# Kernel optimization log

Measured on AMD Instinct MI355X. Metric: run time of the kernel, lower is better.

Reference implementation:

```python
import math
import jax, jax.numpy as jnp
import numpy as np

H, DK = 16, 64            # n_heads, d_kv
NUM_BUCKETS, MAX_DIST = 32, 128


def _relative_position_buckets(S):
    # Bidirectional (encoder) T5 bucketization of relative positions.
    ctx = jnp.arange(S, dtype=jnp.int32)[:, None]      # query positions
    mem = jnp.arange(S, dtype=jnp.int32)[None, :]      # key positions
    rp = mem - ctx                                     # [S, S]
    nb = NUM_BUCKETS // 2
    rb = (rp > 0).astype(jnp.int32) * nb
    n = jnp.abs(rp)
    max_exact = nb // 2
    is_small = n < max_exact
    large = max_exact + (
        jnp.log(jnp.maximum(n, 1).astype(jnp.float32) / max_exact)
        / math.log(MAX_DIST / max_exact)
        * (nb - max_exact)
    ).astype(jnp.int32)
    large = jnp.minimum(large, nb - 1)
    return rb + jnp.where(is_small, n, large)          # [S, S] int32


def setup_inputs() -> dict:
    key = jax.random.key(0)
    ks = jax.random.split(key, 6)
    B, S, D = 4, 1024, 1024
    inner = H * DK
    std = 0.02
    return {
        "hidden_states": jax.random.normal(ks[0], (B, S, D), jnp.float32),
        "Wq": jax.random.normal(ks[1], (inner, D), jnp.float32) * std,
        "Wk": jax.random.normal(ks[2], (inner, D), jnp.float32) * std,
        "Wv": jax.random.normal(ks[3], (inner, D), jnp.float32) * std,
        "Wo": jax.random.normal(ks[4], (D, inner), jnp.float32) * std,
        "rel_bias": jax.random.normal(ks[5], (NUM_BUCKETS, H), jnp.float32) * std,
    }


def reference(hidden_states, Wq, Wk, Wv, Wo, rel_bias):
    B, S, D = hidden_states.shape

    def proj(W):  # bias-free linear + split heads -> [B, H, S, DK]
        return (hidden_states @ W.T).reshape(B, S, H, DK).transpose(0, 2, 1, 3)

    q, k, v = proj(Wq), proj(Wk), proj(Wv)
    # T5: NO 1/sqrt(d) scaling
    scores = jnp.einsum("bhqd,bhkd->bhqk", q, k)       # [B, H, S, S]
    bias = rel_bias[_relative_position_buckets(S)]     # [S, S, H]
    scores = scores + bias.transpose(2, 0, 1)[None]    # broadcast over batch
    attn = jax.nn.softmax(scores, axis=-1)
    ctx = jnp.einsum("bhqk,bhkd->bhqd", attn, v)       # [B, H, S, DK]
    ctx = ctx.transpose(0, 2, 1, 3).reshape(B, S, H * DK)
    return ctx @ Wo.T                                  # [B, S, D]
```

## Files before the change

kernel.cpp:

```cpp
#include <hip/hip_runtime.h>

typedef _Float16 half8 __attribute__((ext_vector_type(8)));
typedef _Float16 half4_t __attribute__((ext_vector_type(4)));
typedef float f32x4 __attribute__((ext_vector_type(4)));

#define GK 1024
#define MEG (1024 * 1024)
#define LOG2E 1.44269504088896f

#define GLD16(gptr, lptr) \
    __builtin_amdgcn_global_load_lds((const __attribute__((address_space(1))) void*)(gptr), \
                                     (__attribute__((address_space(3))) void*)(lptr), 16, 0, 0)

__global__ void cvt_all_kernel(const float* __restrict__ hidden,
                               const float* __restrict__ Wq,
                               const float* __restrict__ Wk,
                               const float* __restrict__ Wv,
                               const float* __restrict__ Wo,
                               _Float16* __restrict__ ws) {
    int b = blockIdx.x;
    const float* src;
    _Float16* dst;
    if (b < 4096)      { src = hidden; dst = ws; }
    else if (b < 5120) { src = Wq; dst = ws + 4 * MEG; b -= 4096; }
    else if (b < 6144) { src = Wk; dst = ws + 5 * MEG; b -= 5120; }
    else if (b < 7168) { src = Wv; dst = ws + 6 * MEG; b -= 6144; }
    else               { src = Wo; dst = ws + 7 * MEG; b -= 7168; }
    int i = (b * 256 + threadIdx.x) * 4;
    f32x4 v = *(const f32x4*)(src + i);
    half4_t h;
    h[0] = (_Float16)v[0]; h[1] = (_Float16)v[1];
    h[2] = (_Float16)v[2]; h[3] = (_Float16)v[3];
    *(half4_t*)(dst + i) = h;
}

__global__ __launch_bounds__(256) void gemm_qkv_kernel(
    const _Float16* __restrict__ A,
    const _Float16* __restrict__ B0,
    const _Float16* __restrict__ B1,
    const _Float16* __restrict__ B2,
    _Float16* __restrict__ O0,
    _Float16* __restrict__ O1,
    _Float16* __restrict__ O2)
{
    int z = blockIdx.z;
    const _Float16* Bw = (z == 0) ? B0 : ((z == 1) ? B1 : B2);
    _Float16* Oh = (z == 0) ? O0 : ((z == 1) ? O1 : O2);

    __shared__ __attribute__((aligned(16))) _Float16 sA[2][128][32];
    __shared__ __attribute__((aligned(16))) _Float16 sB[2][128][32];

    const int tid = threadIdx.x;
    const int wave = tid >> 6, lane = tid & 63;
    const int quad = lane >> 4, l16 = lane & 15;
    const int wr = wave >> 1, wc = wave & 1;
    const int M0 = blockIdx.y * 128, N0 = blockIdx.x * 128;

    const int rl = lane >> 2;
    const int cl = (lane & 3) * 8;
    const size_t aRow0 = (size_t)(M0 + wave * 16 + rl) * GK + cl;
    const size_t aRow1 = aRow0 + (size_t)64 * GK;
    const size_t bRow0 = (size_t)(N0 + wave * 16 + rl) * GK + cl;
    const size_t bRow1 = bRow0 + (size_t)64 * GK;
    _Float16* ldsA[2][2] = {{&sA[0][wave * 16][0], &sA[0][64 + wave * 16][0]},
                            {&sA[1][wave * 16][0], &sA[1][64 + wave * 16][0]}};
    _Float16* ldsB[2][2] = {{&sB[0][wave * 16][0], &sB[0][64 + wave * 16][0]},
                            {&sB[1][wave * 16][0], &sB[1][64 + wave * 16][0]}};

    f32x4 acc[4][4] = {};

    for (int kt = 0; kt < GK / 64; ++kt) {
        const int ko = kt * 64;
        #pragma unroll
        for (int c = 0; c < 2; ++c) {
            GLD16(A + aRow0 + ko + c * 32, ldsA[c][0]);
            GLD16(A + aRow1 + ko + c * 32, ldsA[c][1]);
            GLD16(Bw + bRow0 + ko + c * 32, ldsB[c][0]);
            GLD16(Bw + bRow1 + ko + c * 32, ldsB[c][1]);
        }
        __syncthreads();
        #pragma unroll
        for (int c = 0; c < 2; ++c) {
            half8 af[4], bf[4];
            #pragma unroll
            for (int i = 0; i < 4; ++i)
                af[i] = *(const half8*)&sA[c][wr * 64 + i * 16 + l16][quad * 8];
            #pragma unroll
            for (int j = 0; j < 4; ++j)
                bf[j] = *(const half8*)&sB[c][wc * 64 + j * 16 + l16][quad * 8];
            #pragma unroll
            for (int i = 0; i < 4; ++i)
                #pragma unroll
                for (int j = 0; j < 4; ++j)
                    acc[i][j] = __builtin_amdgcn_mfma_f32_16x16x32_f16(af[i], bf[j], acc[i][j], 0, 0, 0);
        }
        __syncthreads();
    }

    #pragma unroll
    for (int i = 0; i < 4; ++i) {
        #pragma unroll
        for (int j = 0; j < 4; ++j) {
            #pragma unroll
            for (int r = 0; r < 4; ++r) {
                int m = M0 + wr * 64 + i * 16 + quad * 4 + r;
                int n = N0 + wc * 64 + j * 16 + l16;
                int b = m >> 10, s = m & 1023, hh = n >> 6, d = n & 63;
                Oh[((size_t)((b * 16 + hh) * 1024 + s)) * 64 + d] = (_Float16)acc[i][j][r];
            }
        }
    }
}

__global__ __launch_bounds__(256) void gemm_o_kernel(
    const _Float16* __restrict__ A,
    const _Float16* __restrict__ Bw,
    float* __restrict__ Of)
{
    __shared__ __attribute__((aligned(16))) _Float16 sA[2][64][32];
    __shared__ __attribute__((aligned(16))) _Float16 sB[2][128][32];

    const int tid = threadIdx.x;
    const int wave = tid >> 6, lane = tid & 63;
    const int quad = lane >> 4, l16 = lane & 15;
    const int M0 = blockIdx.y * 64, N0 = blockIdx.x * 128;

    const int rl = lane >> 2;
    const int cl = (lane & 3) * 8;
    const size_t aRow  = (size_t)(M0 + wave * 16 + rl) * GK + cl;
    const size_t bRow0 = (size_t)(N0 + wave * 16 + rl) * GK + cl;
    const size_t bRow1 = bRow0 + (size_t)64 * GK;
    _Float16* ldsA[2]    = {&sA[0][wave * 16][0], &sA[1][wave * 16][0]};
    _Float16* ldsB[2][2] = {{&sB[0][wave * 16][0], &sB[0][64 + wave * 16][0]},
                            {&sB[1][wave * 16][0], &sB[1][64 + wave * 16][0]}};

    f32x4 acc[4][2] = {};

    for (int kt = 0; kt < GK / 64; ++kt) {
        const int ko = kt * 64;
        #pragma unroll
        for (int c = 0; c < 2; ++c) {
            GLD16(A + aRow + ko + c * 32, ldsA[c]);
            GLD16(Bw + bRow0 + ko + c * 32, ldsB[c][0]);
            GLD16(Bw + bRow1 + ko + c * 32, ldsB[c][1]);
        }
        __syncthreads();
        #pragma unroll
        for (int c = 0; c < 2; ++c) {
            half8 af[4], bf[2];
            #pragma unroll
            for (int i = 0; i < 4; ++i)
                af[i] = *(const half8*)&sA[c][i * 16 + l16][quad * 8];
            #pragma unroll
            for (int j = 0; j < 2; ++j)
                bf[j] = *(const half8*)&sB[c][wave * 32 + j * 16 + l16][quad * 8];
            #pragma unroll
            for (int i = 0; i < 4; ++i)
                #pragma unroll
                for (int j = 0; j < 2; ++j)
                    acc[i][j] = __builtin_amdgcn_mfma_f32_16x16x32_f16(af[i], bf[j], acc[i][j], 0, 0, 0);
        }
        __syncthreads();
    }

    #pragma unroll
    for (int i = 0; i < 4; ++i) {
        #pragma unroll
        for (int j = 0; j < 2; ++j) {
            #pragma unroll
            for (int r = 0; r < 4; ++r) {
                int m = M0 + i * 16 + quad * 4 + r;
                int n = N0 + wave * 32 + j * 16 + l16;
                Of[(size_t)m * 1024 + n] = acc[i][j][r];
            }
        }
    }
}

__global__ __launch_bounds__(256) void transpose_v_kernel(
    const _Float16* __restrict__ V, _Float16* __restrict__ VT) {
    __shared__ _Float16 tile[64][65];
    const int s0 = blockIdx.x * 64;
    const int bh = blockIdx.y;
    const _Float16* Vb = V + (size_t)bh * 1024 * 64;
    _Float16* Tb = VT + (size_t)bh * 64 * 1024;
    const int tr = threadIdx.x >> 6;
    const int tc = threadIdx.x & 63;
    #pragma unroll
    for (int i = 0; i < 16; ++i) {
        int r = i * 4 + tr;
        tile[r][tc] = Vb[(size_t)(s0 + r) * 64 + tc];
    }
    __syncthreads();
    #pragma unroll
    for (int i = 0; i < 16; ++i) {
        int d = i * 4 + tr;
        Tb[(size_t)d * 1024 + s0 + tc] = tile[tc][d];
    }
}

__global__ __launch_bounds__(256) void attn_kernel(
    const _Float16* __restrict__ Q,
    const _Float16* __restrict__ K,
    const _Float16* __restrict__ VT,
    const float* __restrict__ rel_bias,
    _Float16* __restrict__ ctx)
{
    const int S = 1024;
    const int qt = blockIdx.x;
    const int q0 = qt * 64;
    const int h = blockIdx.y;
    const int b = blockIdx.z;
    const int bh = b * 16 + h;
    const _Float16* Qh = Q + (size_t)bh * S * 64;
    const _Float16* Kh = K + (size_t)bh * S * 64;
    const _Float16* VTh = VT + (size_t)bh * 64 * S;

    __shared__ __attribute__((aligned(16))) _Float16 sQ[64][72];
    __shared__ __attribute__((aligned(16))) _Float16 sK[64][72];
    __shared__ __attribute__((aligned(16))) _Float16 sVt[64][72];
    __shared__ __attribute__((aligned(16))) _Float16 sP[4][16][72];
    __shared__ _Float16 sBias[1088];

    const int tid = threadIdx.x;
    const int wave = tid >> 6, lane = tid & 63;
    const int quad = lane >> 4, l16 = lane & 15;

    {
        int r = tid >> 3, c = (tid & 7) * 8;
        *(half8*)&sQ[r][c]      = *(const half8*)(Qh + (size_t)(q0 + r) * 64 + c);
        *(half8*)&sQ[r + 32][c] = *(const half8*)(Qh + (size_t)(q0 + r + 32) * 64 + c);
    }
    for (int i = tid; i < 1087; i += 256) {
        int delta = i - (q0 + 63);
        int rb = (delta > 0) ? 16 : 0;
        int n = (delta < 0) ? -delta : delta;
        int bucket;
        if (n < 8) bucket = rb + n;
        else bucket = rb + 8 + (n >= 12) + (n >= 16) + (n >= 23) + (n >= 32)
                             + (n >= 46) + (n >= 64) + (n >= 91);
        sBias[i] = (_Float16)rel_bias[bucket * 16 + h];
    }
    __syncthreads();

    half8 qf0 = *(const half8*)&sQ[wave * 16 + l16][quad * 8];
    half8 qf1 = *(const half8*)&sQ[wave * 16 + l16][32 + quad * 8];

    const int sr = tid >> 3;
    const int sc_ = (tid & 7) * 8;
    const _Float16* kp0 = Kh + (size_t)sr * 64 + sc_;
    const _Float16* kp1 = kp0 + (size_t)32 * 64;
    const _Float16* vp0 = VTh + (size_t)sr * S + sc_;
    const _Float16* vp1 = vp0 + (size_t)32 * S;
    _Float16* sKw0 = &sK[sr][sc_];
    _Float16* sKw1 = &sK[sr + 32][sc_];
    _Float16* sVw0 = &sVt[sr][sc_];
    _Float16* sVw1 = &sVt[sr + 32][sc_];

    half8 rk0 = *(const half8*)kp0;
    half8 rk1 = *(const half8*)kp1;
    half8 rv0 = *(const half8*)vp0;
    half8 rv1 = *(const half8*)vp1;
    kp0 += 4096; kp1 += 4096; vp0 += 64; vp1 += 64;

    float m_run = -INFINITY, l_run = 0.0f;
    f32x4 acc[4] = {};

    for (int kt = 0; kt < 16; ++kt) {
        __syncthreads();
        *(half8*)sKw0 = rk0;
        *(half8*)sKw1 = rk1;
        *(half8*)sVw0 = rv0;
        *(half8*)sVw1 = rv1;
        __syncthreads();
        if (kt < 15) {
            rk0 = *(const half8*)kp0;
            rk1 = *(const half8*)kp1;
            rv0 = *(const half8*)vp0;
            rv1 = *(const half8*)vp1;
            kp0 += 4096; kp1 += 4096; vp0 += 64; vp1 += 64;
        }

        f32x4 sc[4] = {};
        #pragma unroll
        for (int j = 0; j < 4; ++j) {
            half8 kf0 = *(const half8*)&sK[j * 16 + l16][quad * 8];
            half8 kf1 = *(const half8*)&sK[j * 16 + l16][32 + quad * 8];
            sc[j] = __builtin_amdgcn_mfma_f32_16x16x32_f16(kf0, qf0, sc[j], 0, 0, 0);
            sc[j] = __builtin_amdgcn_mfma_f32_16x16x32_f16(kf1, qf1, sc[j], 0, 0, 0);
        }

        const int bbase = kt * 64 + quad * 4 - wave * 16 - l16 + 63;
        float ps = 0.0f;
        if (kt <= qt - 3 || kt >= qt + 3) {
            const float cb = (float)sBias[bbase];
            float mx = fmaxf(fmaxf(fmaxf(sc[0][0], sc[0][1]), fmaxf(sc[0][2], sc[0][3])),
                             fmaxf(fmaxf(sc[1][0], sc[1][1]), fmaxf(sc[1][2], sc[1][3])));
            mx = fmaxf(mx, fmaxf(fmaxf(fmaxf(sc[2][0], sc[2][1]), fmaxf(sc[2][2], sc[2][3])),
                                 fmaxf(fmaxf(sc[3][0], sc[3][1]), fmaxf(sc[3][2], sc[3][3]))));
            mx = fmaxf(mx, __shfl_xor(mx, 16));
            mx = fmaxf(mx, __shfl_xor(mx, 32));
            float mnew = fmaxf(m_run, mx + cb);
            float alpha = __expf(m_run - mnew);
            m_run = mnew;
            const float kk = (cb - mnew) * LOG2E;
            #pragma unroll
            for (int j = 0; j < 4; ++j) {
                half4_t pw;
                #pragma unroll
                for (int r = 0; r < 4; ++r) {
                    float p = __builtin_exp2f(__builtin_fmaf(sc[j][r], LOG2E, kk));
                    ps += p;
                    pw[r] = (_Float16)p;
                }
                *(half4_t*)&sP[wave][l16][j * 16 + quad * 4] = pw;
            }
            l_run = l_run * alpha + ps;
            #pragma unroll
            for (int dt = 0; dt < 4; ++dt) acc[dt] *= alpha;
        } else {
            #pragma unroll
            for (int j = 0; j < 4; ++j)
                #pragma unroll
                for (int r = 0; r < 4; ++r)
                    sc[j][r] += (float)sBias[bbase + j * 16 + r];
            float mx = fmaxf(fmaxf(fmaxf(sc[0][0], sc[0][1]), fmaxf(sc[0][2], sc[0][3])),
                             fmaxf(fmaxf(sc[1][0], sc[1][1]), fmaxf(sc[1][2], sc[1][3])));
            mx = fmaxf(mx, fmaxf(fmaxf(fmaxf(sc[2][0], sc[2][1]), fmaxf(sc[2][2], sc[2][3])),
                                 fmaxf(fmaxf(sc[3][0], sc[3][1]), fmaxf(sc[3][2], sc[3][3]))));
            mx = fmaxf(mx, __shfl_xor(mx, 16));
            mx = fmaxf(mx, __shfl_xor(mx, 32));
            float mnew = fmaxf(m_run, mx);
            float alpha = __expf(m_run - mnew);
            m_run = mnew;
            #pragma unroll
            for (int j = 0; j < 4; ++j) {
                half4_t pw;
                #pragma unroll
                for (int r = 0; r < 4; ++r) {
                    float p = __expf(sc[j][r] - mnew);
                    ps += p;
                    pw[r] = (_Float16)p;
                }
                *(half4_t*)&sP[wave][l16][j * 16 + quad * 4] = pw;
            }
            l_run = l_run * alpha + ps;
            #pragma unroll
            for (int dt = 0; dt < 4; ++dt) acc[dt] *= alpha;
        }

        half8 pf0 = *(const half8*)&sP[wave][l16][quad * 8];
        half8 pf1 = *(const half8*)&sP[wave][l16][32 + quad * 8];
        #pragma unroll
        for (int dt = 0; dt < 4; ++dt) {
            half8 vf0 = *(const half8*)&sVt[dt * 16 + l16][quad * 8];
            half8 vf1 = *(const half8*)&sVt[dt * 16 + l16][32 + quad * 8];
            acc[dt] = __builtin_amdgcn_mfma_f32_16x16x32_f16(vf0, pf0, acc[dt], 0, 0, 0);
            acc[dt] = __builtin_amdgcn_mfma_f32_16x16x32_f16(vf1, pf1, acc[dt], 0, 0, 0);
        }
    }

    l_run += __shfl_xor(l_run, 16);
    l_run += __shfl_xor(l_run, 32);
    const float inv = 1.0f / l_run;
    const size_t qg = (size_t)(b * 1024 + q0 + wave * 16 + l16);
    #pragma unroll
    for (int dt = 0; dt < 4; ++dt) {
        half4_t o;
        #pragma unroll
        for (int r = 0; r < 4; ++r) o[r] = (_Float16)(acc[dt][r] * inv);
        *(half4_t*)&ctx[qg * 1024 + h * 64 + dt * 16 + quad * 4] = o;
    }
}

extern "C" void kernel_launch(void* const* d_in, const int* in_sizes, int n_in,
                              void* d_out, int out_size, void* d_ws, size_t ws_size,
                              hipStream_t stream) {
    const float* hidden   = (const float*)d_in[0];
    const float* Wq       = (const float*)d_in[1];
    const float* Wk       = (const float*)d_in[2];
    const float* Wv       = (const float*)d_in[3];
    const float* Wo       = (const float*)d_in[4];
    const float* rel_bias = (const float*)d_in[5];
    float* out = (float*)d_out;

    _Float16* ws    = (_Float16*)d_ws;
    _Float16* h16   = ws;
    _Float16* wq16  = ws + 4 * (size_t)MEG;
    _Float16* wk16  = ws + 5 * (size_t)MEG;
    _Float16* wv16  = ws + 6 * (size_t)MEG;
    _Float16* wo16  = ws + 7 * (size_t)MEG;
    _Float16* Qs    = ws + 8 * (size_t)MEG;
    _Float16* Ks    = ws + 12 * (size_t)MEG;
    _Float16* Vs    = ws + 16 * (size_t)MEG;
    _Float16* ctx16 = ws + 20 * (size_t)MEG;
    _Float16* VTs   = h16;

    cvt_all_kernel<<<8192, 256, 0, stream>>>(hidden, Wq, Wk, Wv, Wo, ws);

    gemm_qkv_kernel<<<dim3(8, 32, 3), 256, 0, stream>>>(
        h16, wq16, wk16, wv16, Qs, Ks, Vs);

    transpose_v_kernel<<<dim3(16, 64), 256, 0, stream>>>(Vs, VTs);

    attn_kernel<<<dim3(16, 16, 4), 256, 0, stream>>>(Qs, Ks, VTs, rel_bias, ctx16);

    gemm_o_kernel<<<dim3(8, 64), 256, 0, stream>>>(ctx16, wo16, out);
}
```

Before: 198.4 us.

## Skip softmax rescale when max stays within threshold; load Q directly; set MFMA priority

Attention now skips the running-max update and accumulator rescale whenever every lane's tile max stays within 8 of the running max (lazy rescaling, as in FA4). This removes the cross-lane shuffles, the exp for alpha and the accumulator multiplies in the common case. Q fragments are loaded straight from global memory into registers, dropping the sQ shared buffer and one barrier. s_setprio is raised around the MFMA blocks to favour the matrix issue of other waves. The exp tree and the partial sums are also restructured to shorten dependency chains. The risk is larger unnormalised exponents, up to about e^8 in fp16 P, which fits fp16 range but slightly changes numerics.

```diff
diff --git a/kernel.cpp b/kernel.cpp
--- a/kernel.cpp
+++ b/kernel.cpp
@@ -199,6 +199,35 @@
     }
 }
 
+#define MAXTREE(mx, s) do {                                          \
+    float t0_ = fmaxf(fmaxf(s[0][0], s[0][1]), s[0][2]);             \
+    float t1_ = fmaxf(fmaxf(s[0][3], s[1][0]), s[1][1]);             \
+    float t2_ = fmaxf(fmaxf(s[1][2], s[1][3]), s[2][0]);             \
+    float t3_ = fmaxf(fmaxf(s[2][1], s[2][2]), s[2][3]);             \
+    float t4_ = fmaxf(fmaxf(s[3][0], s[3][1]), s[3][2]);             \
+    mx = fmaxf(fmaxf(fmaxf(t0_, t1_), fmaxf(t2_, t3_)),              \
+               fmaxf(t4_, s[3][3]));                                 \
+} while (0)
+
+__device__ __forceinline__ float emit_p(const f32x4* sc, float kk,
+                                        _Float16* sProw, int quad) {
+    float ps0 = 0.0f, ps1 = 0.0f;
+    #pragma unroll
+    for (int j = 0; j < 4; ++j) {
+        half4_t pw;
+        float pj = 0.0f;
+        #pragma unroll
+        for (int r = 0; r < 4; ++r) {
+            float p = __builtin_exp2f(__builtin_fmaf(sc[j][r], LOG2E, kk));
+            pj += p;
+            pw[r] = (_Float16)p;
+        }
+        if (j & 1) ps1 += pj; else ps0 += pj;
+        *(half4_t*)&sProw[j * 16 + quad * 4] = pw;
+    }
+    return ps0 + ps1;
+}
+
 __global__ __launch_bounds__(256) void attn_kernel(
     const _Float16* __restrict__ Q,
     const _Float16* __restrict__ K,
@@ -216,7 +245,6 @@
     const _Float16* Kh = K + (size_t)bh * S * 64;
     const _Float16* VTh = VT + (size_t)bh * 64 * S;
 
-    __shared__ __attribute__((aligned(16))) _Float16 sQ[64][72];
     __shared__ __attribute__((aligned(16))) _Float16 sK[64][72];
     __shared__ __attribute__((aligned(16))) _Float16 sVt[64][72];
     __shared__ __attribute__((aligned(16))) _Float16 sP[4][16][72];
@@ -226,11 +254,6 @@
     const int wave = tid >> 6, lane = tid & 63;
     const int quad = lane >> 4, l16 = lane & 15;
 
-    {
-        int r = tid >> 3, c = (tid & 7) * 8;
-        *(half8*)&sQ[r][c]      = *(const half8*)(Qh + (size_t)(q0 + r) * 64 + c);
-        *(half8*)&sQ[r + 32][c] = *(const half8*)(Qh + (size_t)(q0 + r + 32) * 64 + c);
-    }
     for (int i = tid; i < 1087; i += 256) {
         int delta = i - (q0 + 63);
         int rb = (delta > 0) ? 16 : 0;
@@ -241,10 +264,9 @@
                              + (n >= 46) + (n >= 64) + (n >= 91);
         sBias[i] = (_Float16)rel_bias[bucket * 16 + h];
     }
-    __syncthreads();
-
-    half8 qf0 = *(const half8*)&sQ[wave * 16 + l16][quad * 8];
-    half8 qf1 = *(const half8*)&sQ[wave * 16 + l16][32 + quad * 8];
+
+    half8 qf0 = *(const half8*)(Qh + (size_t)(q0 + wave * 16 + l16) * 64 + quad * 8);
+    half8 qf1 = *(const half8*)(Qh + (size_t)(q0 + wave * 16 + l16) * 64 + 32 + quad * 8);
 
     const int sr = tid >> 3;
     const int sc_ = (tid & 7) * 8;
@@ -282,6 +304,7 @@
         }
 
         f32x4 sc[4] = {};
+        __builtin_amdgcn_s_setprio(1);
         #pragma unroll
         for (int j = 0; j < 4; ++j) {
             half8 kf0 = *(const half8*)&sK[j * 16 + l16][quad * 8];
@@ -289,68 +312,50 @@
             sc[j] = __builtin_amdgcn_mfma_f32_16x16x32_f16(kf0, qf0, sc[j], 0, 0, 0);
             sc[j] = __builtin_amdgcn_mfma_f32_16x16x32_f16(kf1, qf1, sc[j], 0, 0, 0);
         }
+        __builtin_amdgcn_s_setprio(0);
 
         const int bbase = kt * 64 + quad * 4 - wave * 16 - l16 + 63;
-        float ps = 0.0f;
         if (kt <= qt - 3 || kt >= qt + 3) {
             const float cb = (float)sBias[bbase];
-            float mx = fmaxf(fmaxf(fmaxf(sc[0][0], sc[0][1]), fmaxf(sc[0][2], sc[0][3])),
-                             fmaxf(fmaxf(sc[1][0], sc[1][1]), fmaxf(sc[1][2], sc[1][3])));
-            mx = fmaxf(mx, fmaxf(fmaxf(fmaxf(sc[2][0], sc[2][1]), fmaxf(sc[2][2], sc[2][3])),
-                                 fmaxf(fmaxf(sc[3][0], sc[3][1]), fmaxf(sc[3][2], sc[3][3]))));
-            mx = fmaxf(mx, __shfl_xor(mx, 16));
-            mx = fmaxf(mx, __shfl_xor(mx, 32));
-            float mnew = fmaxf(m_run, mx + cb);
-            float alpha = __expf(m_run - mnew);
-            m_run = mnew;
-            const float kk = (cb - mnew) * LOG2E;
-            #pragma unroll
-            for (int j = 0; j < 4; ++j) {
-                half4_t pw;
+            float mx; MAXTREE(mx, sc);
+            if (__all(mx + cb <= m_run + 8.0f)) {
+                l_run += emit_p(sc, (cb - m_run) * LOG2E, &sP[wave][l16][0], quad);
+            } else {
+                mx = fmaxf(mx, __shfl_xor(mx, 16));
+                mx = fmaxf(mx, __shfl_xor(mx, 32));
+                float mnew = fmaxf(m_run, mx + cb);
+                float alpha = __expf(m_run - mnew);
+                float ps = emit_p(sc, (cb - mnew) * LOG2E, &sP[wave][l16][0], quad);
+                m_run = mnew;
+                l_run = l_run * alpha + ps;
                 #pragma unroll
-                for (int r = 0; r < 4; ++r) {
-                    float p = __builtin_exp2f(__builtin_fmaf(sc[j][r], LOG2E, kk));
-                    ps += p;
-                    pw[r] = (_Float16)p;
-                }
-                *(half4_t*)&sP[wave][l16][j * 16 + quad * 4] = pw;
+                for (int dt = 0; dt < 4; ++dt) acc[dt] *= alpha;
             }
-            l_run = l_run * alpha + ps;
-            #pragma unroll
-            for (int dt = 0; dt < 4; ++dt) acc[dt] *= alpha;
         } else {
             #pragma unroll
             for (int j = 0; j < 4; ++j)
                 #pragma unroll
                 for (int r = 0; r < 4; ++r)
                     sc[j][r] += (float)sBias[bbase + j * 16 + r];
-            float mx = fmaxf(fmaxf(fmaxf(sc[0][0], sc[0][1]), fmaxf(sc[0][2], sc[0][3])),
-                             fmaxf(fmaxf(sc[1][0], sc[1][1]), fmaxf(sc[1][2], sc[1][3])));
-            mx = fmaxf(mx, fmaxf(fmaxf(fmaxf(sc[2][0], sc[2][1]), fmaxf(sc[2][2], sc[2][3])),
-                                 fmaxf(fmaxf(sc[3][0], sc[3][1]), fmaxf(sc[3][2], sc[3][3]))));
-            mx = fmaxf(mx, __shfl_xor(mx, 16));
-            mx = fmaxf(mx, __shfl_xor(mx, 32));
-            float mnew = fmaxf(m_run, mx);
-            float alpha = __expf(m_run - mnew);
-            m_run = mnew;
-            #pragma unroll
-            for (int j = 0; j < 4; ++j) {
-                half4_t pw;
+            float mx; MAXTREE(mx, sc);
+            if (__all(mx <= m_run + 8.0f)) {
+                l_run += emit_p(sc, -m_run * LOG2E, &sP[wave][l16][0], quad);
+            } else {
+                mx = fmaxf(mx, __shfl_xor(mx, 16));
+                mx = fmaxf(mx, __shfl_xor(mx, 32));
+                float mnew = fmaxf(m_run, mx);
+                float alpha = __expf(m_run - mnew);
+                float ps = emit_p(sc, -mnew * LOG2E, &sP[wave][l16][0], quad);
+                m_run = mnew;
+                l_run = l_run * alpha + ps;
                 #pragma unroll
-                for (int r = 0; r < 4; ++r) {
-                    float p = __expf(sc[j][r] - mnew);
-                    ps += p;
-                    pw[r] = (_Float16)p;
-                }
-                *(half4_t*)&sP[wave][l16][j * 16 + quad * 4] = pw;
+                for (int dt = 0; dt < 4; ++dt) acc[dt] *= alpha;
             }
-            l_run = l_run * alpha + ps;
-            #pragma unroll
-            for (int dt = 0; dt < 4; ++dt) acc[dt] *= alpha;
         }
 
         half8 pf0 = *(const half8*)&sP[wave][l16][quad * 8];
         half8 pf1 = *(const half8*)&sP[wave][l16][32 + quad * 8];
+        __builtin_amdgcn_s_setprio(1);
         #pragma unroll
         for (int dt = 0; dt < 4; ++dt) {
             half8 vf0 = *(const half8*)&sVt[dt * 16 + l16][quad * 8];
@@ -358,6 +363,7 @@
             acc[dt] = __builtin_amdgcn_mfma_f32_16x16x32_f16(vf0, pf0, acc[dt], 0, 0, 0);
             acc[dt] = __builtin_amdgcn_mfma_f32_16x16x32_f16(vf1, pf1, acc[dt], 0, 0, 0);
         }
+        __builtin_amdgcn_s_setprio(0);
     }
 
     l_run += __shfl_xor(l_run, 16);
```

Result: slower. 205.2 us (+3.4%).

## Fuse V transpose into QKV GEMM epilogue and remap blocks per XCD

Applied to the files above, without the earlier changes.

The QKV GEMM now writes V straight into the transposed [b,h,d,s] layout with 4-wide half stores, so the separate transpose_v kernel and its launch and round trip through memory are gone. Both GEMMs switch to a 1-D grid whose block IDs are remapped so that consecutive blocks on the same XCD share A rows. The aim is better L2 reuse on the multi-die MI355X. The transposed V store is strided by 1024 halves per lane, which may write less efficiently than the row-major store.

```diff
diff --git a/kernel.cpp b/kernel.cpp
--- a/kernel.cpp
+++ b/kernel.cpp
@@ -43,7 +43,13 @@
     _Float16* __restrict__ O1,
     _Float16* __restrict__ O2)
 {
-    int z = blockIdx.z;
+    const int lid = blockIdx.x;
+    const int xcd = lid & 7;
+    const int rr = lid >> 3;
+    const int xb = rr & 7;
+    const int gg = xcd * 12 + (rr >> 3);
+    const int yb = gg & 31;
+    const int z  = gg >> 5;
     const _Float16* Bw = (z == 0) ? B0 : ((z == 1) ? B1 : B2);
     _Float16* Oh = (z == 0) ? O0 : ((z == 1) ? O1 : O2);
 
@@ -54,7 +60,7 @@
     const int wave = tid >> 6, lane = tid & 63;
     const int quad = lane >> 4, l16 = lane & 15;
     const int wr = wave >> 1, wc = wave & 1;
-    const int M0 = blockIdx.y * 128, N0 = blockIdx.x * 128;
+    const int M0 = yb * 128, N0 = xb * 128;
 
     const int rl = lane >> 2;
     const int cl = (lane & 3) * 8;
@@ -97,16 +103,32 @@
         __syncthreads();
     }
 
-    #pragma unroll
-    for (int i = 0; i < 4; ++i) {
-        #pragma unroll
-        for (int j = 0; j < 4; ++j) {
-            #pragma unroll
-            for (int r = 0; r < 4; ++r) {
-                int m = M0 + wr * 64 + i * 16 + quad * 4 + r;
+    if (z == 2) {
+        #pragma unroll
+        for (int i = 0; i < 4; ++i) {
+            #pragma unroll
+            for (int j = 0; j < 4; ++j) {
+                int m = M0 + wr * 64 + i * 16 + quad * 4;
                 int n = N0 + wc * 64 + j * 16 + l16;
                 int b = m >> 10, s = m & 1023, hh = n >> 6, d = n & 63;
-                Oh[((size_t)((b * 16 + hh) * 1024 + s)) * 64 + d] = (_Float16)acc[i][j][r];
+                half4_t o;
+                #pragma unroll
+                for (int r = 0; r < 4; ++r) o[r] = (_Float16)acc[i][j][r];
+                *(half4_t*)&Oh[((size_t)((b * 16 + hh) * 64 + d)) * 1024 + s] = o;
+            }
+        }
+    } else {
+        #pragma unroll
+        for (int i = 0; i < 4; ++i) {
+            #pragma unroll
+            for (int j = 0; j < 4; ++j) {
+                #pragma unroll
+                for (int r = 0; r < 4; ++r) {
+                    int m = M0 + wr * 64 + i * 16 + quad * 4 + r;
+                    int n = N0 + wc * 64 + j * 16 + l16;
+                    int b = m >> 10, s = m & 1023, hh = n >> 6, d = n & 63;
+                    Oh[((size_t)((b * 16 + hh) * 1024 + s)) * 64 + d] = (_Float16)acc[i][j][r];
+                }
             }
         }
     }
@@ -117,13 +139,19 @@
     const _Float16* __restrict__ Bw,
     float* __restrict__ Of)
 {
+    const int lid = blockIdx.x;
+    const int xcd = lid & 7;
+    const int rr = lid >> 3;
+    const int xb = rr & 7;
+    const int yb = xcd * 8 + (rr >> 3);
+
     __shared__ __attribute__((aligned(16))) _Float16 sA[2][64][32];
     __shared__ __attribute__((aligned(16))) _Float16 sB[2][128][32];
 
     const int tid = threadIdx.x;
     const int wave = tid >> 6, lane = tid & 63;
     const int quad = lane >> 4, l16 = lane & 15;
-    const int M0 = blockIdx.y * 64, N0 = blockIdx.x * 128;
+    const int M0 = yb * 64, N0 = xb * 128;
 
     const int rl = lane >> 2;
     const int cl = (lane & 3) * 8;
@@ -174,28 +202,6 @@
                 Of[(size_t)m * 1024 + n] = acc[i][j][r];
             }
         }
-    }
-}
-
-__global__ __launch_bounds__(256) void transpose_v_kernel(
-    const _Float16* __restrict__ V, _Float16* __restrict__ VT) {
-    __shared__ _Float16 tile[64][65];
-    const int s0 = blockIdx.x * 64;
-    const int bh = blockIdx.y;
-    const _Float16* Vb = V + (size_t)bh * 1024 * 64;
-    _Float16* Tb = VT + (size_t)bh * 64 * 1024;
-    const int tr = threadIdx.x >> 6;
-    const int tc = threadIdx.x & 63;
-    #pragma unroll
-    for (int i = 0; i < 16; ++i) {
-        int r = i * 4 + tr;
-        tile[r][tc] = Vb[(size_t)(s0 + r) * 64 + tc];
-    }
-    __syncthreads();
-    #pragma unroll
-    for (int i = 0; i < 16; ++i) {
-        int d = i * 4 + tr;
-        Tb[(size_t)d * 1024 + s0 + tc] = tile[tc][d];
     }
 }
 
@@ -392,18 +398,15 @@
     _Float16* wo16  = ws + 7 * (size_t)MEG;
     _Float16* Qs    = ws + 8 * (size_t)MEG;
     _Float16* Ks    = ws + 12 * (size_t)MEG;
-    _Float16* Vs    = ws + 16 * (size_t)MEG;
+    _Float16* VTs   = ws + 16 * (size_t)MEG;
     _Float16* ctx16 = ws + 20 * (size_t)MEG;
-    _Float16* VTs   = h16;
 
     cvt_all_kernel<<<8192, 256, 0, stream>>>(hidden, Wq, Wk, Wv, Wo, ws);
 
-    gemm_qkv_kernel<<<dim3(8, 32, 3), 256, 0, stream>>>(
-        h16, wq16, wk16, wv16, Qs, Ks, Vs);
-
-    transpose_v_kernel<<<dim3(16, 64), 256, 0, stream>>>(Vs, VTs);
+    gemm_qkv_kernel<<<dim3(768), 256, 0, stream>>>(
+        h16, wq16, wk16, wv16, Qs, Ks, VTs);
 
     attn_kernel<<<dim3(16, 16, 4), 256, 0, stream>>>(Qs, Ks, VTs, rel_bias, ctx16);
 
-    gemm_o_kernel<<<dim3(8, 64), 256, 0, stream>>>(ctx16, wo16, out);
+    gemm_o_kernel<<<dim3(512), 256, 0, stream>>>(ctx16, wo16, out);
 }
```

Measured after the change: 191.6 us. 1.04x faster.
